# Kernel tuning notes

Hardware: AMD Instinct MI355X
Metric: run time of the kernel (lower is better)

The kernel has to match this reference:

```python
import jax, jax.numpy as jnp
import numpy as np

N_NODES = 100000
N_EDGES = 3200000
IN_F, HID, N_CLS = 1433, 16, 7


def setup_inputs() -> dict:
    key = jax.random.key(0)
    ks = jax.random.split(key, 6)
    return {
        "x": jax.random.normal(ks[0], (N_NODES, IN_F), dtype=jnp.float32),
        "W1": jax.random.normal(ks[1], (IN_F, HID), dtype=jnp.float32) * 0.02,
        "b1": jax.random.normal(ks[2], (HID,), dtype=jnp.float32) * 0.02,
        "W2": jax.random.normal(ks[3], (HID, N_CLS), dtype=jnp.float32) * 0.1,
        "b2": jax.random.normal(ks[4], (N_CLS,), dtype=jnp.float32) * 0.1,
        "edge_index": jax.random.randint(ks[5], (2, N_EDGES), 0, N_NODES, dtype=jnp.int64),
    }


def _gcn_layer(h, W, b, row, col, n_nodes):
    # dense linear
    h = h @ W + b
    # symmetric degree normalization (self-loops already appended)
    deg = jax.ops.segment_sum(jnp.ones_like(col, dtype=h.dtype), col, num_segments=n_nodes)
    dinv = deg ** -0.5
    norm = dinv[row] * dinv[col]  # [E]
    # gather-scale-scatter message passing (aggr='add', source row -> target col)
    msgs = norm[:, None] * h[row]  # [E, F_out]
    return jax.ops.segment_sum(msgs, col, num_segments=n_nodes)


def reference(x, W1, b1, W2, b2, edge_index):
    n = x.shape[0]
    self_loops = jnp.broadcast_to(jnp.arange(n, dtype=edge_index.dtype)[None, :], (2, n))
    ei = jnp.concatenate([edge_index, self_loops], axis=1)
    row, col = ei[0], ei[1]
    h = jax.nn.relu(_gcn_layer(x, W1, b1, row, col, n))
    h = jax.nn.relu(_gcn_layer(h, W2, b2, row, col, n))
    return jax.nn.log_softmax(h, axis=1)
```

## Files before the change

### kernel.cpp

```cpp
#include <hip/hip_runtime.h>
#include <math.h>

constexpr int K_IN  = 1433;
constexpr int HID   = 16;
constexpr int NCLS  = 7;
constexpr int BLK   = 256;
constexpr int CHUNK = 256;
constexpr int KP    = 260;
constexpr int NB    = 256;
constexpr int NBLKA = 1024;

__device__ inline float4 wave_reduce4(float4 v) {
#pragma unroll
  for (int off = 32; off > 0; off >>= 1) {
    v.x += __shfl_xor(v.x, off);
    v.y += __shfl_xor(v.y, off);
    v.z += __shfl_xor(v.z, off);
    v.w += __shfl_xor(v.w, off);
  }
  return v;
}

__device__ inline int block_excl_scan256(int v, int* wsum) {
  const int lane = threadIdx.x & 63, wid = threadIdx.x >> 6;
  int s = v;
#pragma unroll
  for (int off = 1; off < 64; off <<= 1) {
    int t = __shfl_up(s, off);
    if (lane >= off) s += t;
  }
  if (lane == 63) wsum[wid] = s;
  __syncthreads();
  int woff = 0;
#pragma unroll
  for (int k = 0; k < 4; ++k) woff += (k < wid) ? wsum[k] : 0;
  return woff + s - v;
}


__global__ __launch_bounds__(256) void k_histA(const int* __restrict__ col,
                                               int* __restrict__ gHist, int nE) {
  __shared__ int h[NB];
  h[threadIdx.x] = 0;
  __syncthreads();
  const int ch = (nE + NBLKA - 1) / NBLKA;
  const int e0 = blockIdx.x * ch;
  const int e1 = min(e0 + ch, nE);
  for (int e = e0 + threadIdx.x; e < e1; e += 256) atomicAdd(&h[col[e] >> 9], 1);
  __syncthreads();
  gHist[threadIdx.x * NBLKA + blockIdx.x] = h[threadIdx.x];
}

__global__ __launch_bounds__(256) void k_scanA(int* __restrict__ gHist,
                                               int* __restrict__ bTot) {
  __shared__ int wsum[4];
  const int b = blockIdx.x, t = threadIdx.x;
  int4* p = (int4*)(gHist + (size_t)b * NBLKA);
  int4 c = p[t];
  const int tsum = c.x + c.y + c.z + c.w;
  const int base = block_excl_scan256(tsum, wsum);
  int4 o; o.x = base; o.y = base + c.x; o.z = o.y + c.y; o.w = o.z + c.z;
  p[t] = o;
  if (t == 255) bTot[b] = base + tsum;
}

__global__ __launch_bounds__(256) void k_placeA(const int* __restrict__ row,
                                                const int* __restrict__ col,
                                                const int* __restrict__ gHist,
                                                const int* __restrict__ bTot,
                                                int* __restrict__ sorted, int nE) {
  __shared__ int cur[NB];
  __shared__ int wsum[4];
  const int t = threadIdx.x;
  const int excl = block_excl_scan256(bTot[t], wsum);
  cur[t] = excl + gHist[t * NBLKA + blockIdx.x];
  __syncthreads();
  const int ch = (nE + NBLKA - 1) / NBLKA;
  const int e0 = blockIdx.x * ch;
  const int e1 = min(e0 + ch, nE);
  for (int e = e0 + t; e < e1; e += 256) {
    const int c = col[e];
    const int p = atomicAdd(&cur[c >> 9], 1);
    sorted[p] = ((c & 511) << 17) | row[e];
  }
}

__global__ __launch_bounds__(256) void k_bucketB(const int* __restrict__ sorted,
                                                 const int* __restrict__ bTot,
                                                 int* __restrict__ cnt,
                                                 int* __restrict__ start,
                                                 float* __restrict__ dinv,
                                                 int* __restrict__ rows, int n) {
  __shared__ int h[512];
  __shared__ int ls[512];
  __shared__ int sBase[NB];
  __shared__ int wsum[4];
  const int b = blockIdx.x, t = threadIdx.x;
  const int lane = t & 63, wid = t >> 6;
  h[t] = 0; h[t + 256] = 0;
  sBase[t] = block_excl_scan256(bTot[t], wsum);
  __syncthreads();
  const int s0 = sBase[b];
  const int s1 = (b < 255) ? sBase[b + 1] : s0 + bTot[b];
  for (int e = s0 + t; e < s1; e += 256) atomicAdd(&h[(sorted[e] >> 17) & 511], 1);
  __syncthreads();
  const int c0 = h[2 * t], c1 = h[2 * t + 1];
  const int tsum = c0 + c1;
  int s = tsum;
#pragma unroll
  for (int off = 1; off < 64; off <<= 1) { int v = __shfl_up(s, off); if (lane >= off) s += v; }
  if (lane == 63) wsum[wid] = s;
  __syncthreads();
  int woff = 0;
#pragma unroll
  for (int k = 0; k < 4; ++k) woff += (k < wid) ? wsum[k] : 0;
  const int base = woff + s - tsum;
  ls[2 * t] = base;
  ls[2 * t + 1] = base + c0;
  const int gc0 = b * 512 + 2 * t;
  if (gc0 < n) {
    cnt[gc0] = c0; start[gc0] = s0 + base;
    dinv[gc0] = rsqrtf((float)(c0 + 1));
  }
  if (gc0 + 1 < n) {
    cnt[gc0 + 1] = c1; start[gc0 + 1] = s0 + base + c0;
    dinv[gc0 + 1] = rsqrtf((float)(c1 + 1));
  }
  __syncthreads();
  for (int e = s0 + t; e < s1; e += 256) {
    const int rc = sorted[e];
    const int p = atomicAdd(&ls[(rc >> 17) & 511], 1);
    rows[s0 + p] = rc & 0x1FFFF;
  }
}


__global__ __launch_bounds__(BLK) void k_gemm1(const float* __restrict__ x,
                                               const float* __restrict__ W1,
                                               const float* __restrict__ b1,
                                               const float* __restrict__ dinv,
                                               float* __restrict__ h1s, int n) {
  __shared__ float wt[HID][KP];
  const int lane = threadIdx.x & 63;
  const int wave = threadIdx.x >> 6;
  const int r0 = blockIdx.x * 8 + wave * 2;
  const int r1 = r0 + 1;
  const bool v0 = r0 < n, v1 = r1 < n;
  const float* xr0 = x + (size_t)r0 * K_IN;
  const float* xr1 = x + (size_t)r1 * K_IN;
  float acc0[HID] = {};
  float acc1[HID] = {};

  for (int kc = 0; kc < K_IN; kc += CHUNK) {
    const int kcnt = min(CHUNK, K_IN - kc);
    for (int t = threadIdx.x; t < kcnt * 4; t += BLK) {
      const int kk = t >> 2, f4 = t & 3;
      const float4 v = ((const float4*)W1)[(size_t)(kc + kk) * 4 + f4];
      wt[f4 * 4 + 0][kk] = v.x;
      wt[f4 * 4 + 1][kk] = v.y;
      wt[f4 * 4 + 2][kk] = v.z;
      wt[f4 * 4 + 3][kk] = v.w;
    }
    __syncthreads();

    const int k0 = lane * 4;
    float4 x0 = make_float4(0.f, 0.f, 0.f, 0.f);
    float4 x1 = make_float4(0.f, 0.f, 0.f, 0.f);
    if (kcnt == CHUNK) {
      if (v0) x0 = *(const float4*)(xr0 + kc + k0);
      if (v1) x1 = *(const float4*)(xr1 + kc + k0);
    } else if (k0 < kcnt) {
      float t0[4] = {0.f, 0.f, 0.f, 0.f}, t1[4] = {0.f, 0.f, 0.f, 0.f};
#pragma unroll
      for (int i = 0; i < 4; ++i) {
        if (k0 + i < kcnt) {
          if (v0) t0[i] = xr0[kc + k0 + i];
          if (v1) t1[i] = xr1[kc + k0 + i];
        }
      }
      x0 = make_float4(t0[0], t0[1], t0[2], t0[3]);
      x1 = make_float4(t1[0], t1[1], t1[2], t1[3]);
    }
    const bool live = (k0 < kcnt);
#pragma unroll
    for (int f = 0; f < HID; ++f) {
      if (live) {
        const float4 w = *(const float4*)&wt[f][k0];
        acc0[f] = fmaf(x0.x, w.x, fmaf(x0.y, w.y, fmaf(x0.z, w.z, fmaf(x0.w, w.w, acc0[f]))));
        acc1[f] = fmaf(x1.x, w.x, fmaf(x1.y, w.y, fmaf(x1.z, w.z, fmaf(x1.w, w.w, acc1[f]))));
      }
    }
    __syncthreads();
  }

  float4 a0[4], a1[4];
#pragma unroll
  for (int f4 = 0; f4 < 4; ++f4) {
    a0[f4] = wave_reduce4(make_float4(acc0[f4 * 4], acc0[f4 * 4 + 1], acc0[f4 * 4 + 2], acc0[f4 * 4 + 3]));
    a1[f4] = wave_reduce4(make_float4(acc1[f4 * 4], acc1[f4 * 4 + 1], acc1[f4 * 4 + 2], acc1[f4 * 4 + 3]));
  }
  if (lane == 0) {
    const float4* b14 = (const float4*)b1;
    const float d0 = v0 ? dinv[r0] : 0.0f;
    const float d1 = v1 ? dinv[r1] : 0.0f;
    float4* o0 = (float4*)(h1s + (size_t)r0 * HID);
    float4* o1 = (float4*)(h1s + (size_t)r1 * HID);
#pragma unroll
    for (int f4 = 0; f4 < 4; ++f4) {
      const float4 bb = b14[f4];
      if (v0) o0[f4] = make_float4(d0 * (a0[f4].x + bb.x), d0 * (a0[f4].y + bb.y),
                                   d0 * (a0[f4].z + bb.z), d0 * (a0[f4].w + bb.w));
      if (v1) o1[f4] = make_float4(d1 * (a1[f4].x + bb.x), d1 * (a1[f4].y + bb.y),
                                   d1 * (a1[f4].z + bb.z), d1 * (a1[f4].w + bb.w));
    }
  }
}

__global__ __launch_bounds__(BLK) void k_gather1g2(const int* __restrict__ rows,
                                                   const int* __restrict__ start,
                                                   const int* __restrict__ cnt,
                                                   const float* __restrict__ dinv,
                                                   const float* __restrict__ h1s,
                                                   const float* __restrict__ W2,
                                                   const float* __restrict__ b2,
                                                   float* __restrict__ h2s, int n) {
  __shared__ float w2s[HID * NCLS];
  __shared__ float b2s[NCLS];
  if (threadIdx.x < HID * NCLS) w2s[threadIdx.x] = W2[threadIdx.x];
  if (threadIdx.x < NCLS) b2s[threadIdx.x] = b2[threadIdx.x];
  __syncthreads();
  const int node = blockIdx.x * 4 + (threadIdx.x >> 6);
  const int lane = threadIdx.x & 63;
  const int f = lane & 15;
  const int g = lane >> 4;
  if (node >= n) return;
  const float dc = dinv[node];
  float acc = (g == 0) ? h1s[(size_t)node * HID + f] : 0.0f;
  const int m = cnt[node];
  const int* bp = rows + start[node];
  int q = g;
  for (; q + 4 < m; q += 8) {
    const int r0 = bp[q], r1 = bp[q + 4];
    acc += h1s[(size_t)r0 * HID + f];
    acc += h1s[(size_t)r1 * HID + f];
  }
  if (q < m) acc += h1s[(size_t)bp[q] * HID + f];
  acc += __shfl_xor(acc, 16);
  acc += __shfl_xor(acc, 32);
  acc = fmaxf(dc * acc, 0.0f);
  float sj[NCLS];
#pragma unroll
  for (int j = 0; j < NCLS; ++j) sj[j] = acc * w2s[f * NCLS + j];
#pragma unroll
  for (int off = 1; off < 16; off <<= 1)
#pragma unroll
    for (int j = 0; j < NCLS; ++j) sj[j] += __shfl_xor(sj[j], off);
  if (g == 0 && f < NCLS) {
    float v = sj[0];
#pragma unroll
    for (int j = 1; j < NCLS; ++j) if (f == j) v = sj[j];
    h2s[(size_t)node * NCLS + f] = dc * (v + b2s[f]);
  }
}

__global__ __launch_bounds__(BLK) void k_gather2(const int* __restrict__ rows,
                                                 const int* __restrict__ start,
                                                 const int* __restrict__ cnt,
                                                 const float* __restrict__ dinv,
                                                 const float* __restrict__ h2s,
                                                 float* __restrict__ out, int n) {
  const int node = blockIdx.x * 4 + (threadIdx.x >> 6);
  const int lane = threadIdx.x & 63;
  const int f = lane & 7;
  const int g = lane >> 3;
  if (node >= n) return;
  const float dc = dinv[node];
  float acc = (g == 0) ? h2s[(size_t)node * NCLS + f] : 0.0f;
  const int m = cnt[node];
  const int* bp = rows + start[node];
  int q = g;
  for (; q + 8 < m; q += 16) {
    const int r0 = bp[q], r1 = bp[q + 8];
    acc += h2s[(size_t)r0 * NCLS + f];
    acc += h2s[(size_t)r1 * NCLS + f];
  }
  if (q < m) acc += h2s[(size_t)bp[q] * NCLS + f];
  acc += __shfl_xor(acc, 8);
  acc += __shfl_xor(acc, 16);
  acc += __shfl_xor(acc, 32);
  const bool act = f < NCLS;
  const float t = fmaxf(dc * acc, 0.0f);
  float tm = act ? t : -1e30f;
#pragma unroll
  for (int off = 1; off < 8; off <<= 1) tm = fmaxf(tm, __shfl_xor(tm, off, 8));
  float se = act ? __expf(t - tm) : 0.0f;
#pragma unroll
  for (int off = 1; off < 8; off <<= 1) se += __shfl_xor(se, off, 8);
  const float lse = tm + __logf(se);
  if (g == 0 && act) out[(size_t)node * NCLS + f] = t - lse;
}

extern "C" void kernel_launch(void* const* d_in, const int* in_sizes, int n_in,
                              void* d_out, int out_size, void* d_ws, size_t ws_size,
                              hipStream_t stream) {
  const float* x  = (const float*)d_in[0];
  const float* W1 = (const float*)d_in[1];
  const float* b1 = (const float*)d_in[2];
  const float* W2 = (const float*)d_in[3];
  const float* b2 = (const float*)d_in[4];
  const int*   ei = (const int*)d_in[5];

  const int n  = in_sizes[0] / K_IN;
  const int nE = in_sizes[5] / 2;
  const int* row = ei;
  const int* col = ei + nE;

  char* w = (char*)d_ws;
  size_t off = 0;
  auto alloc = [&](size_t elems) {
    void* p = w + off;
    off += ((elems * 4 + 15) & ~(size_t)15);
    return p;
  };
  int*   cnt    = (int*)alloc(n);
  int*   start  = (int*)alloc(n);
  float* dinv   = (float*)alloc(n);
  float* h1s    = (float*)alloc((size_t)n * HID);
  float* h2s    = (float*)alloc((size_t)n * NCLS + 16);
  int*   gHist  = (int*)alloc((size_t)NB * NBLKA);
  int*   bTot   = (int*)alloc(NB);
  int*   sorted = (int*)alloc(nE);
  int*   rows   = (int*)alloc(nE);

  const int gG1 = (n + 7) / 8;
  const int gWN = (n + 3) / 4;

  k_histA<<<NBLKA, 256, 0, stream>>>(col, gHist, nE);
  k_scanA<<<NB, 256, 0, stream>>>(gHist, bTot);
  k_placeA<<<NBLKA, 256, 0, stream>>>(row, col, gHist, bTot, sorted, nE);
  k_bucketB<<<NB, 256, 0, stream>>>(sorted, bTot, cnt, start, dinv, rows, n);

  k_gemm1<<<gG1, BLK, 0, stream>>>(x, W1, b1, dinv, h1s, n);
  k_gather1g2<<<gWN, BLK, 0, stream>>>(rows, start, cnt, dinv, h1s, W2, b2, h2s, n);

  k_gather2<<<gWN, BLK, 0, stream>>>(rows, start, cnt, dinv, h2s, (float*)d_out, n);
}
```

Measured before the change: 458.5 us.

## Make first-layer GEMM persistent with all of W1 resident in LDS

The x·W1 kernel now launches a fixed grid of 256 blocks of 512 threads. Each block stages the whole transposed W1, zero-padded to 1536, into shared memory once, then loops over row pairs with a grid stride. Each wave issues all six x chunks for its two rows up front before doing the FMAs. This removes the per-chunk W1 reloads and barriers. The cost is one large-LDS block per CU and lower occupancy, which may limit how much memory traffic is in flight for this bandwidth-bound read of x.

```diff
diff --git a/kernel.cpp b/kernel.cpp
--- a/kernel.cpp
+++ b/kernel.cpp
@@ -5,8 +5,7 @@
 constexpr int HID   = 16;
 constexpr int NCLS  = 7;
 constexpr int BLK   = 256;
-constexpr int CHUNK = 256;
-constexpr int KP    = 260;
+constexpr int KP2   = 1536;
 constexpr int NB    = 256;
 constexpr int NBLKA = 1024;
 
@@ -135,83 +134,93 @@
 }
 
 
-__global__ __launch_bounds__(BLK) void k_gemm1(const float* __restrict__ x,
+__global__ __launch_bounds__(512) void k_gemm1(const float* __restrict__ x,
                                                const float* __restrict__ W1,
                                                const float* __restrict__ b1,
                                                const float* __restrict__ dinv,
                                                float* __restrict__ h1s, int n) {
-  __shared__ float wt[HID][KP];
-  const int lane = threadIdx.x & 63;
-  const int wave = threadIdx.x >> 6;
-  const int r0 = blockIdx.x * 8 + wave * 2;
-  const int r1 = r0 + 1;
-  const bool v0 = r0 < n, v1 = r1 < n;
-  const float* xr0 = x + (size_t)r0 * K_IN;
-  const float* xr1 = x + (size_t)r1 * K_IN;
-  float acc0[HID] = {};
-  float acc1[HID] = {};
-
-  for (int kc = 0; kc < K_IN; kc += CHUNK) {
-    const int kcnt = min(CHUNK, K_IN - kc);
-    for (int t = threadIdx.x; t < kcnt * 4; t += BLK) {
-      const int kk = t >> 2, f4 = t & 3;
-      const float4 v = ((const float4*)W1)[(size_t)(kc + kk) * 4 + f4];
-      wt[f4 * 4 + 0][kk] = v.x;
-      wt[f4 * 4 + 1][kk] = v.y;
-      wt[f4 * 4 + 2][kk] = v.z;
-      wt[f4 * 4 + 3][kk] = v.w;
-    }
-    __syncthreads();
-
-    const int k0 = lane * 4;
-    float4 x0 = make_float4(0.f, 0.f, 0.f, 0.f);
-    float4 x1 = make_float4(0.f, 0.f, 0.f, 0.f);
-    if (kcnt == CHUNK) {
-      if (v0) x0 = *(const float4*)(xr0 + kc + k0);
-      if (v1) x1 = *(const float4*)(xr1 + kc + k0);
-    } else if (k0 < kcnt) {
+  __shared__ float wt[HID][KP2];
+  const int tid = threadIdx.x;
+  const int lane = tid & 63;
+  const int wave = tid >> 6;
+
+  for (int t = tid; t < K_IN * 4; t += 512) {
+    const int kk = t >> 2, f4 = t & 3;
+    const float4 v = ((const float4*)W1)[(size_t)kk * 4 + f4];
+    wt[f4 * 4 + 0][kk] = v.x;
+    wt[f4 * 4 + 1][kk] = v.y;
+    wt[f4 * 4 + 2][kk] = v.z;
+    wt[f4 * 4 + 3][kk] = v.w;
+  }
+  for (int t = tid; t < HID * (KP2 - K_IN); t += 512) {
+    const int f = t / (KP2 - K_IN);
+    wt[f][K_IN + t % (KP2 - K_IN)] = 0.0f;
+  }
+  __syncthreads();
+
+  const int npairs = (n + 1) / 2;
+  const int gw = blockIdx.x * 8 + wave;
+  const int k0 = lane * 4;
+
+  for (int pair = gw; pair < npairs; pair += 2048) {
+    const int r0 = pair * 2;
+    const int r1 = r0 + 1;
+    const bool v1 = r1 < n;
+    const float* xr0 = x + (size_t)r0 * K_IN;
+    const float* xr1 = x + (size_t)r1 * K_IN;
+
+    float4 x0[6], x1[6];
+#pragma unroll
+    for (int c = 0; c < 5; ++c) {
+      x0[c] = *(const float4*)(xr0 + c * 256 + k0);
+      x1[c] = v1 ? *(const float4*)(xr1 + c * 256 + k0) : make_float4(0.f, 0.f, 0.f, 0.f);
+    }
+    {
+      const int kb = 5 * 256 + k0;
       float t0[4] = {0.f, 0.f, 0.f, 0.f}, t1[4] = {0.f, 0.f, 0.f, 0.f};
 #pragma unroll
       for (int i = 0; i < 4; ++i) {
-        if (k0 + i < kcnt) {
-          if (v0) t0[i] = xr0[kc + k0 + i];
-          if (v1) t1[i] = xr1[kc + k0 + i];
+        if (kb + i < K_IN) {
+          t0[i] = xr0[kb + i];
+          if (v1) t1[i] = xr1[kb + i];
         }
       }
-      x0 = make_float4(t0[0], t0[1], t0[2], t0[3]);
-      x1 = make_float4(t1[0], t1[1], t1[2], t1[3]);
-    }
-    const bool live = (k0 < kcnt);
-#pragma unroll
-    for (int f = 0; f < HID; ++f) {
-      if (live) {
-        const float4 w = *(const float4*)&wt[f][k0];
-        acc0[f] = fmaf(x0.x, w.x, fmaf(x0.y, w.y, fmaf(x0.z, w.z, fmaf(x0.w, w.w, acc0[f]))));
-        acc1[f] = fmaf(x1.x, w.x, fmaf(x1.y, w.y, fmaf(x1.z, w.z, fmaf(x1.w, w.w, acc1[f]))));
+      x0[5] = make_float4(t0[0], t0[1], t0[2], t0[3]);
+      x1[5] = make_float4(t1[0], t1[1], t1[2], t1[3]);
+    }
+
+    float acc0[HID] = {};
+    float acc1[HID] = {};
+#pragma unroll
+    for (int c = 0; c < 6; ++c) {
+#pragma unroll
+      for (int f = 0; f < HID; ++f) {
+        const float4 w = *(const float4*)&wt[f][c * 256 + k0];
+        acc0[f] = fmaf(x0[c].x, w.x, fmaf(x0[c].y, w.y, fmaf(x0[c].z, w.z, fmaf(x0[c].w, w.w, acc0[f]))));
+        acc1[f] = fmaf(x1[c].x, w.x, fmaf(x1[c].y, w.y, fmaf(x1[c].z, w.z, fmaf(x1[c].w, w.w, acc1[f]))));
       }
     }
-    __syncthreads();
-  }
-
-  float4 a0[4], a1[4];
-#pragma unroll
-  for (int f4 = 0; f4 < 4; ++f4) {
-    a0[f4] = wave_reduce4(make_float4(acc0[f4 * 4], acc0[f4 * 4 + 1], acc0[f4 * 4 + 2], acc0[f4 * 4 + 3]));
-    a1[f4] = wave_reduce4(make_float4(acc1[f4 * 4], acc1[f4 * 4 + 1], acc1[f4 * 4 + 2], acc1[f4 * 4 + 3]));
-  }
-  if (lane == 0) {
-    const float4* b14 = (const float4*)b1;
-    const float d0 = v0 ? dinv[r0] : 0.0f;
-    const float d1 = v1 ? dinv[r1] : 0.0f;
-    float4* o0 = (float4*)(h1s + (size_t)r0 * HID);
-    float4* o1 = (float4*)(h1s + (size_t)r1 * HID);
+
+    float4 a0[4], a1[4];
 #pragma unroll
     for (int f4 = 0; f4 < 4; ++f4) {
-      const float4 bb = b14[f4];
-      if (v0) o0[f4] = make_float4(d0 * (a0[f4].x + bb.x), d0 * (a0[f4].y + bb.y),
-                                   d0 * (a0[f4].z + bb.z), d0 * (a0[f4].w + bb.w));
-      if (v1) o1[f4] = make_float4(d1 * (a1[f4].x + bb.x), d1 * (a1[f4].y + bb.y),
-                                   d1 * (a1[f4].z + bb.z), d1 * (a1[f4].w + bb.w));
+      a0[f4] = wave_reduce4(make_float4(acc0[f4 * 4], acc0[f4 * 4 + 1], acc0[f4 * 4 + 2], acc0[f4 * 4 + 3]));
+      a1[f4] = wave_reduce4(make_float4(acc1[f4 * 4], acc1[f4 * 4 + 1], acc1[f4 * 4 + 2], acc1[f4 * 4 + 3]));
+    }
+    if (lane == 0) {
+      const float4* b14 = (const float4*)b1;
+      const float d0 = dinv[r0];
+      const float d1 = v1 ? dinv[r1] : 0.0f;
+      float4* o0 = (float4*)(h1s + (size_t)r0 * HID);
+      float4* o1 = (float4*)(h1s + (size_t)r1 * HID);
+#pragma unroll
+      for (int f4 = 0; f4 < 4; ++f4) {
+        const float4 bb = b14[f4];
+        o0[f4] = make_float4(d0 * (a0[f4].x + bb.x), d0 * (a0[f4].y + bb.y),
+                             d0 * (a0[f4].z + bb.z), d0 * (a0[f4].w + bb.w));
+        if (v1) o1[f4] = make_float4(d1 * (a1[f4].x + bb.x), d1 * (a1[f4].y + bb.y),
+                                     d1 * (a1[f4].z + bb.z), d1 * (a1[f4].w + bb.w));
+      }
     }
   }
 }
@@ -332,7 +341,6 @@
   int*   sorted = (int*)alloc(nE);
   int*   rows   = (int*)alloc(nE);
 
-  const int gG1 = (n + 7) / 8;
   const int gWN = (n + 3) / 4;
 
   k_histA<<<NBLKA, 256, 0, stream>>>(col, gHist, nE);
@@ -340,7 +348,7 @@
   k_placeA<<<NBLKA, 256, 0, stream>>>(row, col, gHist, bTot, sorted, nE);
   k_bucketB<<<NB, 256, 0, stream>>>(sorted, bTot, cnt, start, dinv, rows, n);
 
-  k_gemm1<<<gG1, BLK, 0, stream>>>(x, W1, b1, dinv, h1s, n);
+  k_gemm1<<<256, 512, 0, stream>>>(x, W1, b1, dinv, h1s, n);
   k_gather1g2<<<gWN, BLK, 0, stream>>>(rows, start, cnt, dinv, h1s, W2, b2, h2s, n);
 
   k_gather2<<<gWN, BLK, 0, stream>>>(rows, start, cnt, dinv, h2s, (float*)d_out, n);
```

Result: slower. 1.384 ms (+201.8%).

## Locally sort edge tiles in LDS before scattering to bucket positions

Applied to the files above, without the earlier changes.

The bucket placement kernel now handles edges in tiles of 1024. Each tile is counting-sorted by bucket in shared memory, then written out so that consecutive threads write contiguous runs within each bucket. The aim is to replace random single-word global scatters with more coalesced writes and fewer contended shared atomics, at the cost of extra shared memory, barriers and a scan per tile. Separately, the live check in the dense GEMM loop is hoisted out of the unrolled feature loop.

```diff
diff --git a/kernel.cpp b/kernel.cpp
--- a/kernel.cpp
+++ b/kernel.cpp
@@ -9,6 +9,7 @@
 constexpr int KP    = 260;
 constexpr int NB    = 256;
 constexpr int NBLKA = 1024;
+constexpr int TILE  = 1024;
 
 __device__ inline float4 wave_reduce4(float4 v) {
 #pragma unroll
@@ -70,18 +71,55 @@
                                                 const int* __restrict__ bTot,
                                                 int* __restrict__ sorted, int nE) {
   __shared__ int cur[NB];
+  __shared__ int th[NB];
+  __shared__ int tofs[NB];
+  __shared__ int tlocC[TILE];
+  __shared__ int tlocR[TILE];
   __shared__ int wsum[4];
   const int t = threadIdx.x;
   const int excl = block_excl_scan256(bTot[t], wsum);
   cur[t] = excl + gHist[t * NBLKA + blockIdx.x];
-  __syncthreads();
   const int ch = (nE + NBLKA - 1) / NBLKA;
   const int e0 = blockIdx.x * ch;
   const int e1 = min(e0 + ch, nE);
-  for (int e = e0 + t; e < e1; e += 256) {
-    const int c = col[e];
-    const int p = atomicAdd(&cur[c >> 9], 1);
-    sorted[p] = ((c & 511) << 17) | row[e];
+
+  for (int ts = e0; ts < e1; ts += TILE) {
+    const int cnt = min(TILE, e1 - ts);
+    th[t] = 0;
+    __syncthreads();
+    int myc[4], myr[4], slot[4];
+#pragma unroll
+    for (int j = 0; j < 4; ++j) {
+      const int e = ts + t + j * 256;
+      if (e - ts < cnt) {
+        myc[j] = col[e];
+        myr[j] = row[e];
+        slot[j] = atomicAdd(&th[myc[j] >> 9], 1);
+      } else myc[j] = -1;
+    }
+    __syncthreads();
+    const int myofs = block_excl_scan256(th[t], wsum);
+    tofs[t] = myofs;
+    __syncthreads();
+#pragma unroll
+    for (int j = 0; j < 4; ++j)
+      if (myc[j] >= 0) {
+        const int p = tofs[myc[j] >> 9] + slot[j];
+        tlocC[p] = myc[j];
+        tlocR[p] = myr[j];
+      }
+    __syncthreads();
+#pragma unroll
+    for (int j = 0; j < 4; ++j) {
+      const int idx = t + j * 256;
+      if (idx < cnt) {
+        const int c = tlocC[idx];
+        const int b = c >> 9;
+        sorted[cur[b] + (idx - tofs[b])] = ((c & 511) << 17) | tlocR[idx];
+      }
+    }
+    __syncthreads();
+    cur[t] += th[t];
   }
 }
 
@@ -182,9 +220,9 @@
       x1 = make_float4(t1[0], t1[1], t1[2], t1[3]);
     }
     const bool live = (k0 < kcnt);
-#pragma unroll
-    for (int f = 0; f < HID; ++f) {
-      if (live) {
+    if (live) {
+#pragma unroll
+      for (int f = 0; f < HID; ++f) {
         const float4 w = *(const float4*)&wt[f][k0];
         acc0[f] = fmaf(x0.x, w.x, fmaf(x0.y, w.y, fmaf(x0.z, w.z, fmaf(x0.w, w.w, acc0[f]))));
         acc1[f] = fmaf(x1.x, w.x, fmaf(x1.y, w.y, fmaf(x1.z, w.z, fmaf(x1.w, w.w, acc1[f]))));
```

Result: slower. 476.3 us (+3.9%).

## Drop LDS staging of W1 in gemm1 and read weights directly from cache

Applied to the files above, without the earlier changes.

Removes the shared-memory transposed copy of W1 and the per-chunk block barriers in the first dense layer. Each lane now walks K with a stride of 64, loading one scalar of x per row and four float4 of W1 straight from global memory. Barriers and the LDS footprint go away, but x is read with scalar 4-byte coalesced loads instead of float4, and the 92KB of W1 is re-read by every block through L1/L2.

```diff
diff --git a/kernel.cpp b/kernel.cpp
--- a/kernel.cpp
+++ b/kernel.cpp
@@ -5,8 +5,6 @@
 constexpr int HID   = 16;
 constexpr int NCLS  = 7;
 constexpr int BLK   = 256;
-constexpr int CHUNK = 256;
-constexpr int KP    = 260;
 constexpr int NB    = 256;
 constexpr int NBLKA = 1024;
 
@@ -140,7 +138,6 @@
                                                const float* __restrict__ b1,
                                                const float* __restrict__ dinv,
                                                float* __restrict__ h1s, int n) {
-  __shared__ float wt[HID][KP];
   const int lane = threadIdx.x & 63;
   const int wave = threadIdx.x >> 6;
   const int r0 = blockIdx.x * 8 + wave * 2;
@@ -151,46 +148,51 @@
   float acc0[HID] = {};
   float acc1[HID] = {};
 
-  for (int kc = 0; kc < K_IN; kc += CHUNK) {
-    const int kcnt = min(CHUNK, K_IN - kc);
-    for (int t = threadIdx.x; t < kcnt * 4; t += BLK) {
-      const int kk = t >> 2, f4 = t & 3;
-      const float4 v = ((const float4*)W1)[(size_t)(kc + kk) * 4 + f4];
-      wt[f4 * 4 + 0][kk] = v.x;
-      wt[f4 * 4 + 1][kk] = v.y;
-      wt[f4 * 4 + 2][kk] = v.z;
-      wt[f4 * 4 + 3][kk] = v.w;
-    }
-    __syncthreads();
-
-    const int k0 = lane * 4;
-    float4 x0 = make_float4(0.f, 0.f, 0.f, 0.f);
-    float4 x1 = make_float4(0.f, 0.f, 0.f, 0.f);
-    if (kcnt == CHUNK) {
-      if (v0) x0 = *(const float4*)(xr0 + kc + k0);
-      if (v1) x1 = *(const float4*)(xr1 + kc + k0);
-    } else if (k0 < kcnt) {
-      float t0[4] = {0.f, 0.f, 0.f, 0.f}, t1[4] = {0.f, 0.f, 0.f, 0.f};
-#pragma unroll
-      for (int i = 0; i < 4; ++i) {
-        if (k0 + i < kcnt) {
-          if (v0) t0[i] = xr0[kc + k0 + i];
-          if (v1) t1[i] = xr1[kc + k0 + i];
-        }
-      }
-      x0 = make_float4(t0[0], t0[1], t0[2], t0[3]);
-      x1 = make_float4(t1[0], t1[1], t1[2], t1[3]);
-    }
-    const bool live = (k0 < kcnt);
-#pragma unroll
-    for (int f = 0; f < HID; ++f) {
-      if (live) {
-        const float4 w = *(const float4*)&wt[f][k0];
-        acc0[f] = fmaf(x0.x, w.x, fmaf(x0.y, w.y, fmaf(x0.z, w.z, fmaf(x0.w, w.w, acc0[f]))));
-        acc1[f] = fmaf(x1.x, w.x, fmaf(x1.y, w.y, fmaf(x1.z, w.z, fmaf(x1.w, w.w, acc1[f]))));
+  constexpr int NSTEP = (K_IN + 63) / 64;
+#pragma unroll 2
+  for (int s = 0; s < NSTEP - 1; ++s) {
+    const int k = s * 64 + lane;
+    const float4* wp = (const float4*)(W1 + (size_t)k * HID);
+    const float4 w0 = wp[0], w1 = wp[1], w2 = wp[2], w3 = wp[3];
+    const float xv0 = v0 ? xr0[k] : 0.0f;
+    const float xv1 = v1 ? xr1[k] : 0.0f;
+    acc0[0]  = fmaf(xv0, w0.x, acc0[0]);  acc1[0]  = fmaf(xv1, w0.x, acc1[0]);
+    acc0[1]  = fmaf(xv0, w0.y, acc0[1]);  acc1[1]  = fmaf(xv1, w0.y, acc1[1]);
+    acc0[2]  = fmaf(xv0, w0.z, acc0[2]);  acc1[2]  = fmaf(xv1, w0.z, acc1[2]);
+    acc0[3]  = fmaf(xv0, w0.w, acc0[3]);  acc1[3]  = fmaf(xv1, w0.w, acc1[3]);
+    acc0[4]  = fmaf(xv0, w1.x, acc0[4]);  acc1[4]  = fmaf(xv1, w1.x, acc1[4]);
+    acc0[5]  = fmaf(xv0, w1.y, acc0[5]);  acc1[5]  = fmaf(xv1, w1.y, acc1[5]);
+    acc0[6]  = fmaf(xv0, w1.z, acc0[6]);  acc1[6]  = fmaf(xv1, w1.z, acc1[6]);
+    acc0[7]  = fmaf(xv0, w1.w, acc0[7]);  acc1[7]  = fmaf(xv1, w1.w, acc1[7]);
+    acc0[8]  = fmaf(xv0, w2.x, acc0[8]);  acc1[8]  = fmaf(xv1, w2.x, acc1[8]);
+    acc0[9]  = fmaf(xv0, w2.y, acc0[9]);  acc1[9]  = fmaf(xv1, w2.y, acc1[9]);
+    acc0[10] = fmaf(xv0, w2.z, acc0[10]); acc1[10] = fmaf(xv1, w2.z, acc1[10]);
+    acc0[11] = fmaf(xv0, w2.w, acc0[11]); acc1[11] = fmaf(xv1, w2.w, acc1[11]);
+    acc0[12] = fmaf(xv0, w3.x, acc0[12]); acc1[12] = fmaf(xv1, w3.x, acc1[12]);
+    acc0[13] = fmaf(xv0, w3.y, acc0[13]); acc1[13] = fmaf(xv1, w3.y, acc1[13]);
+    acc0[14] = fmaf(xv0, w3.z, acc0[14]); acc1[14] = fmaf(xv1, w3.z, acc1[14]);
+    acc0[15] = fmaf(xv0, w3.w, acc0[15]); acc1[15] = fmaf(xv1, w3.w, acc1[15]);
+  }
+  {
+    const int k = (NSTEP - 1) * 64 + lane;
+    if (k < K_IN) {
+      const float4* wp = (const float4*)(W1 + (size_t)k * HID);
+      const float4 w0 = wp[0], w1 = wp[1], w2 = wp[2], w3 = wp[3];
+      const float xv0 = v0 ? xr0[k] : 0.0f;
+      const float xv1 = v1 ? xr1[k] : 0.0f;
+      const float4 ww[4] = {w0, w1, w2, w3};
+#pragma unroll
+      for (int f4 = 0; f4 < 4; ++f4) {
+        acc0[f4 * 4 + 0] = fmaf(xv0, ww[f4].x, acc0[f4 * 4 + 0]);
+        acc0[f4 * 4 + 1] = fmaf(xv0, ww[f4].y, acc0[f4 * 4 + 1]);
+        acc0[f4 * 4 + 2] = fmaf(xv0, ww[f4].z, acc0[f4 * 4 + 2]);
+        acc0[f4 * 4 + 3] = fmaf(xv0, ww[f4].w, acc0[f4 * 4 + 3]);
+        acc1[f4 * 4 + 0] = fmaf(xv1, ww[f4].x, acc1[f4 * 4 + 0]);
+        acc1[f4 * 4 + 1] = fmaf(xv1, ww[f4].y, acc1[f4 * 4 + 1]);
+        acc1[f4 * 4 + 2] = fmaf(xv1, ww[f4].z, acc1[f4 * 4 + 2]);
+        acc1[f4 * 4 + 3] = fmaf(xv1, ww[f4].w, acc1[f4 * 4 + 3]);
       }
     }
-    __syncthreads();
   }
 
   float4 a0[4], a1[4];
```

Measured after the change: 540.3 us. 1.18x slower.
